# Performance work log

Measured on AMD Instinct MI355X. Metric: run time of the kernel, lower is better.

The kernel has to match this reference:

```python
import jax, jax.numpy as jnp
import numpy as np

E = 20000       # num edges (nodes of the edge-adjacency graph)
FDIM = 128      # edge_feature_dim
D = 16          # stalk_dim ('diagonal' => mlp output dim = D)
P = 300000      # number of adjacent (i, j) pairs extracted from L1
EPS = 1e-5      # LayerNorm eps


def _xavier(key, fan_in, fan_out):
    lim = np.sqrt(6.0 / (fan_in + fan_out)).astype(np.float32)
    return jax.random.uniform(key, (fan_in, fan_out), jnp.float32, -lim, lim)


def _layernorm(x, g, b):
    mu = jnp.mean(x, axis=-1, keepdims=True)
    var = jnp.mean((x - mu) ** 2, axis=-1, keepdims=True)
    return (x - mu) * jax.lax.rsqrt(var + EPS) * g + b


def setup_inputs() -> dict:
    key = jax.random.key(0)
    ks = jax.random.split(key, 8)
    return {
        "edge_features": jax.random.normal(ks[0], (E, FDIM), jnp.float32),
        "pair_i": jax.random.randint(ks[1], (P,), 0, E),
        "pair_j": jax.random.randint(ks[2], (P,), 0, E),
        # MLP: Linear(2F,64) -> LN -> ReLU -> Linear(64,32) -> LN -> ReLU -> Linear(32,D)
        "W1": _xavier(ks[3], 2 * FDIM, 64), "b1": jnp.zeros((64,), jnp.float32),
        "g1": jnp.ones((64,), jnp.float32), "be1": jnp.zeros((64,), jnp.float32),
        "W2": _xavier(ks[4], 64, 32), "b2": jnp.zeros((32,), jnp.float32),
        "g2": jnp.ones((32,), jnp.float32), "be2": jnp.zeros((32,), jnp.float32),
        "W3": _xavier(ks[5], 32, D), "b3": jnp.zeros((D,), jnp.float32),
    }


def reference(edge_features, pair_i, pair_j, W1, b1, g1, be1, W2, b2, g2, be2, W3, b3):
    # Gather the two edge feature vectors per adjacent pair and concat: [P, 2F]
    x = jnp.concatenate([edge_features[pair_i], edge_features[pair_j]], axis=1)
    h = jax.nn.relu(_layernorm(x @ W1 + b1, g1, be1))      # [P, 64]
    h = jax.nn.relu(_layernorm(h @ W2 + b2, g2, be2))      # [P, 32]
    params = h @ W3 + b3                                    # [P, D]
    # diagonal sheaf: F_ij = diag(params) for every pair, batched (diag_embed)
    return params[:, :, None] * jnp.eye(D, dtype=params.dtype)  # [P, D, D]
```

## Files before the change

### kernel.cpp

```cpp
#include <hip/hip_runtime.h>

__global__ void bad_map_marker(float* out) {
    if (threadIdx.x == 0 && blockIdx.x == 0) out[0] = 1.0e6f;
}

__device__ __forceinline__ void mlp_tail_compute(float* h, float* pr, int D,
        const float* g1, const float* be1,
        const float* W2, const float* b2,
        const float* g2, const float* be2,
        const float* W3, const float* b3) {
    float s = 0.f, ss = 0.f;
    #pragma unroll
    for (int d = 0; d < 64; ++d) { s += h[d]; ss += h[d] * h[d]; }
    float mu  = s * (1.f / 64.f);
    float inv = rsqrtf(ss * (1.f / 64.f) - mu * mu + 1e-5f);
    #pragma unroll
    for (int d = 0; d < 64; ++d)
        h[d] = fmaxf((h[d] - mu) * inv * g1[d] + be1[d], 0.f);

    float a2[32];
    const float4* w2v = (const float4*)W2;
    #pragma unroll
    for (int n = 0; n < 32; ++n) a2[n] = b2[n];
    for (int k = 0; k < 64; ++k) {
        float hk = h[k];
        #pragma unroll
        for (int q = 0; q < 8; ++q) {
            float4 w = w2v[k * 8 + q];
            a2[4 * q + 0] += hk * w.x;
            a2[4 * q + 1] += hk * w.y;
            a2[4 * q + 2] += hk * w.z;
            a2[4 * q + 3] += hk * w.w;
        }
    }
    s = 0.f; ss = 0.f;
    #pragma unroll
    for (int n = 0; n < 32; ++n) { s += a2[n]; ss += a2[n] * a2[n]; }
    mu  = s * (1.f / 32.f);
    inv = rsqrtf(ss * (1.f / 32.f) - mu * mu + 1e-5f);
    #pragma unroll
    for (int n = 0; n < 32; ++n)
        a2[n] = fmaxf((a2[n] - mu) * inv * g2[n] + be2[n], 0.f);

    for (int d = 0; d < D; ++d) pr[d] = b3[d];
    for (int k = 0; k < 32; ++k) {
        float hk = a2[k];
        const float* wr = W3 + k * D;
        for (int d = 0; d < D; ++d) pr[d] += hk * wr[d];
    }
}

__device__ __forceinline__ void store_diag16_f32_256(const float* pp, float* out, int P) {
    const int t = threadIdx.x;
    float4* outv = (float4*)out + (size_t)blockIdx.x * 16384;
    const int pbase = blockIdx.x * 256;
    #pragma unroll 8
    for (int it = 0; it < 64; ++it) {
        int g = it * 256 + t;
        int pl = g >> 6;
        int rem = g & 63;
        int d = rem >> 2;
        int c4 = rem & 3;
        float val = pp[pl * 17 + d];
        bool on = (d >> 2) == c4;
        float4 v;
        v.x = (on && (d & 3) == 0) ? val : 0.f;
        v.y = (on && (d & 3) == 1) ? val : 0.f;
        v.z = (on && (d & 3) == 2) ? val : 0.f;
        v.w = (on && (d & 3) == 3) ? val : 0.f;
        if (pbase + pl < P) outv[g] = v;
    }
}

__global__ __launch_bounds__(256)
void precompute_y(const float* __restrict__ ef, const float* __restrict__ W1,
                  const float* __restrict__ b1, float* __restrict__ Y, int E) {
    __shared__ __align__(16) float el[64 * 132];
    const int t = threadIdx.x;
    const int ebase = blockIdx.x * 64;

    for (int idx = t; idx < 2048; idx += 256) {
        int er = idx >> 5, ec = idx & 31;
        if (ebase + er < E)
            *((float4*)(el + er * 132) + ec) =
                *((const float4*)(ef + (size_t)(ebase + er) * 128) + ec);
    }
    __syncthreads();

    const int cg = t & 15;
    const int eg = t >> 4;
    const int half = cg >> 3;
    const int col64 = (cg & 7) * 8;

    float acc[4][8];
    #pragma unroll
    for (int i = 0; i < 4; ++i)
        #pragma unroll
        for (int c = 0; c < 8; ++c) acc[i][c] = 0.f;

    const float* wbase = W1 + (size_t)half * 128 * 64 + col64;
    #pragma unroll 4
    for (int k = 0; k < 128; ++k) {
        float4 w0 = *(const float4*)(wbase + (size_t)k * 64);
        float4 w1 = *(const float4*)(wbase + (size_t)k * 64 + 4);
        float wv[8] = {w0.x, w0.y, w0.z, w0.w, w1.x, w1.y, w1.z, w1.w};
        #pragma unroll
        for (int i = 0; i < 4; ++i) {
            float a = el[(eg * 4 + i) * 132 + k];
            #pragma unroll
            for (int c = 0; c < 8; ++c) acc[i][c] += a * wv[c];
        }
    }

    float bb[8];
    #pragma unroll
    for (int c = 0; c < 8; ++c) bb[c] = (half == 0) ? b1[col64 + c] : 0.f;
    #pragma unroll
    for (int i = 0; i < 4; ++i) {
        int e = ebase + eg * 4 + i;
        if (e < E) {
            float* dst = Y + (size_t)e * 128 + half * 64 + col64;
            #pragma unroll
            for (int c = 0; c < 8; ++c) dst[c] = acc[i][c] + bb[c];
        }
    }
}

__global__ __launch_bounds__(256)
void sheaf_pairs(const int* __restrict__ pi, const int* __restrict__ pj,
                 const float* __restrict__ Y,
                 const float* __restrict__ g1, const float* __restrict__ be1,
                 const float* __restrict__ W2, const float* __restrict__ b2,
                 const float* __restrict__ g2, const float* __restrict__ be2,
                 const float* __restrict__ W3, const float* __restrict__ b3,
                 float* __restrict__ out, int P) {
    __shared__ float pp[256 * 17];
    __shared__ __align__(16) float w2s[64 * 32];
    __shared__ __align__(16) float w3s[32 * 16];
    __shared__ float g1s[64], be1s[64], b2s[32], g2s[32], be2s[32], b3s[16];

    const int t = threadIdx.x;
    int p = blockIdx.x * 256 + t;
    int pc = p < P ? p : P - 1;
    int i = pi[pc], j = pj[pc];
    const float4* y1 = (const float4*)(Y + (size_t)i * 128);
    const float4* y2 = (const float4*)(Y + (size_t)j * 128 + 64);
    float h[64];
    #pragma unroll
    for (int q = 0; q < 16; ++q) {
        float4 a = y1[q], b = y2[q];
        h[4 * q + 0] = a.x + b.x;
        h[4 * q + 1] = a.y + b.y;
        h[4 * q + 2] = a.z + b.z;
        h[4 * q + 3] = a.w + b.w;
    }

    {
        const float4* s2 = (const float4*)W2;
        float4* d2 = (float4*)w2s;
        d2[t]       = s2[t];
        d2[t + 256] = s2[t + 256];
        if (t < 128) ((float4*)w3s)[t] = ((const float4*)W3)[t];
        if (t < 64)                 { g1s[t] = g1[t]; be1s[t] = be1[t]; }
        else if (t < 96)            b2s[t - 64]   = b2[t - 64];
        else if (t < 128)           g2s[t - 96]   = g2[t - 96];
        else if (t < 160)           be2s[t - 128] = be2[t - 128];
        else if (t < 176)           b3s[t - 160]  = b3[t - 160];
    }
    __syncthreads();

    float pr[16];
    mlp_tail_compute(h, pr, 16, g1s, be1s, w2s, b2s, g2s, be2s, w3s, b3s);
    #pragma unroll
    for (int d = 0; d < 16; ++d) pp[t * 17 + d] = pr[d];
    __syncthreads();
    store_diag16_f32_256(pp, out, P);
}

__global__ __launch_bounds__(256)
void sheaf_generic(const float* __restrict__ ef,
                   const int* __restrict__ pi, const int* __restrict__ pj,
                   const float* __restrict__ W1, const float* __restrict__ b1,
                   const float* __restrict__ g1, const float* __restrict__ be1,
                   const float* __restrict__ W2, const float* __restrict__ b2,
                   const float* __restrict__ g2, const float* __restrict__ be2,
                   const float* __restrict__ W3, const float* __restrict__ b3,
                   float* __restrict__ out, int P, int F, int D) {
    __shared__ float pp[256 * 17];
    int p = blockIdx.x * 256 + threadIdx.x;
    int pc = p < P ? p : P - 1;
    int i = pi[pc], j = pj[pc];
    const float* efi = ef + (size_t)i * F;
    const float* efj = ef + (size_t)j * F;
    float h[64];
    #pragma unroll
    for (int n = 0; n < 64; ++n) h[n] = b1[n];
    for (int k = 0; k < F; ++k) {
        float ei = efi[k];
        float ej = efj[k];
        const float* wi = W1 + (size_t)k * 64;
        const float* wj = W1 + (size_t)(F + k) * 64;
        #pragma unroll
        for (int n = 0; n < 64; ++n) h[n] += ei * wi[n] + ej * wj[n];
    }
    float pr[32];
    mlp_tail_compute(h, pr, D, g1, be1, W2, b2, g2, be2, W3, b3);

    if (D == 16) {
        #pragma unroll
        for (int d = 0; d < 16; ++d) pp[threadIdx.x * 17 + d] = pr[d];
        __syncthreads();
        store_diag16_f32_256(pp, out, P);
    } else {
        if (p < P) {
            float* po = out + (size_t)p * D * D;
            for (int r = 0; r < D; ++r) {
                float dv = pr[r];
                for (int c = 0; c < D; ++c) po[r * D + c] = (r == c) ? dv : 0.f;
            }
        }
    }
}

struct Map { int ef, pi, pj, w1, b1, g1, be1, w2, b2, g2, be2, w3, b3; };

static bool validate_map(const Map& m, const int* s, int n_in, long out_size,
                         int* Fo, int* Eo, int* Do, int* Po) {
    if (n_in < 13) return false;
    if (s[m.b1] != 64 || s[m.g1] != 64 || s[m.be1] != 64) return false;
    if (s[m.b2] != 32 || s[m.g2] != 32 || s[m.be2] != 32) return false;
    if (s[m.w2] != 64 * 32) return false;
    long w1 = s[m.w1];
    if (w1 <= 0 || (w1 % 128) != 0) return false;
    long F = w1 / 128;
    if (F <= 0) return false;
    int D = s[m.b3];
    if (D <= 0 || D > 32) return false;
    if (s[m.w3] != 32 * D) return false;
    long P = s[m.pi];
    if (P <= 0 || s[m.pj] != P) return false;
    long ef = s[m.ef];
    if (ef <= 0 || (ef % F) != 0) return false;
    long E = ef / F;
    if (out_size != P * D * D) return false;
    *Fo = (int)F; *Eo = (int)E; *Do = D; *Po = (int)P;
    return true;
}

extern "C" void kernel_launch(void* const* d_in, const int* in_sizes, int n_in,
                              void* d_out, int out_size, void* d_ws, size_t ws_size,
                              hipStream_t stream) {
    const Map pos   = {0, 1, 2, 3, 4, 5, 6, 7, 8, 9, 10, 11, 12};
    const Map alpha = {8, 11, 12, 0, 3, 9, 6, 1, 4, 10, 7, 2, 5};

    int F = 0, E = 0, D = 0, P = 0;
    Map m;
    if (validate_map(pos, in_sizes, n_in, (long)out_size, &F, &E, &D, &P)) {
        m = pos;
    } else if (validate_map(alpha, in_sizes, n_in, (long)out_size, &F, &E, &D, &P)) {
        m = alpha;
    } else {
        bad_map_marker<<<dim3(1), dim3(64), 0, stream>>>((float*)d_out);
        return;
    }

    const float* ef  = (const float*)d_in[m.ef];
    const int*   pi  = (const int*)d_in[m.pi];
    const int*   pj  = (const int*)d_in[m.pj];
    const float* W1  = (const float*)d_in[m.w1];
    const float* b1  = (const float*)d_in[m.b1];
    const float* g1  = (const float*)d_in[m.g1];
    const float* be1 = (const float*)d_in[m.be1];
    const float* W2  = (const float*)d_in[m.w2];
    const float* b2  = (const float*)d_in[m.b2];
    const float* g2  = (const float*)d_in[m.g2];
    const float* be2 = (const float*)d_in[m.be2];
    const float* W3  = (const float*)d_in[m.w3];
    const float* b3  = (const float*)d_in[m.b3];
    float* out = (float*)d_out;

    const size_t y_bytes = (size_t)E * 128 * 4;

    if (F == 128 && D == 16 && ws_size >= y_bytes) {
        float* Y = (float*)d_ws;
        precompute_y<<<dim3((E + 63) / 64), dim3(256), 0, stream>>>(ef, W1, b1, Y, E);
        sheaf_pairs<<<dim3((P + 255) / 256), dim3(256), 0, stream>>>(
            pi, pj, Y, g1, be1, W2, b2, g2, be2, W3, b3, out, P);
    } else {
        sheaf_generic<<<dim3((P + 255) / 256), dim3(256), 0, stream>>>(
            ef, pi, pj, W1, b1, g1, be1, W2, b2, g2, be2, W3, b3, out, P, F, D);
    }
}
```

Before: 389.4 us.

## Split each pair's MLP across four threads with shuffle reductions

Replaces the one-thread-per-pair MLP tail with a four-threads-per-pair layout. Each lane handles a 16-wide slice of the hidden layer and its part of the second matmul (against a transposed W2 in shared memory), and the partial sums and LayerNorm statistics are combined with XOR shuffles. Each lane then computes four outputs of the final layer, and the diagonal output is written as float4 stores. This cuts per-thread register pressure and raises occupancy and memory-level parallelism. In exchange it duplicates the second LayerNorm across lanes, adds shuffle traffic, and reloads the weight setup in four times as many blocks.

```diff
diff --git a/kernel.cpp b/kernel.cpp
--- a/kernel.cpp
+++ b/kernel.cpp
@@ -126,55 +126,118 @@
     }
 }
 
-__global__ __launch_bounds__(256)
-void sheaf_pairs(const int* __restrict__ pi, const int* __restrict__ pj,
-                 const float* __restrict__ Y,
-                 const float* __restrict__ g1, const float* __restrict__ be1,
-                 const float* __restrict__ W2, const float* __restrict__ b2,
-                 const float* __restrict__ g2, const float* __restrict__ be2,
-                 const float* __restrict__ W3, const float* __restrict__ b3,
-                 float* __restrict__ out, int P) {
-    __shared__ float pp[256 * 17];
-    __shared__ __align__(16) float w2s[64 * 32];
+__global__ __launch_bounds__(256, 4)
+void sheaf_pairs_quad(const int* __restrict__ pi, const int* __restrict__ pj,
+                      const float* __restrict__ Y,
+                      const float* __restrict__ g1, const float* __restrict__ be1,
+                      const float* __restrict__ W2, const float* __restrict__ b2,
+                      const float* __restrict__ g2, const float* __restrict__ be2,
+                      const float* __restrict__ W3, const float* __restrict__ b3,
+                      float* __restrict__ out, int P) {
+    __shared__ __align__(16) float w2t[32 * 64];
     __shared__ __align__(16) float w3s[32 * 16];
+    __shared__ __align__(16) float pp[64 * 20];
     __shared__ float g1s[64], be1s[64], b2s[32], g2s[32], be2s[32], b3s[16];
 
-    const int t = threadIdx.x;
-    int p = blockIdx.x * 256 + t;
+    const int t  = threadIdx.x;
+    const int pl = t >> 2;
+    const int q  = t & 3;
+    const int pbase = blockIdx.x * 64;
+    int p  = pbase + pl;
     int pc = p < P ? p : P - 1;
     int i = pi[pc], j = pj[pc];
-    const float4* y1 = (const float4*)(Y + (size_t)i * 128);
-    const float4* y2 = (const float4*)(Y + (size_t)j * 128 + 64);
-    float h[64];
-    #pragma unroll
-    for (int q = 0; q < 16; ++q) {
-        float4 a = y1[q], b = y2[q];
-        h[4 * q + 0] = a.x + b.x;
-        h[4 * q + 1] = a.y + b.y;
-        h[4 * q + 2] = a.z + b.z;
-        h[4 * q + 3] = a.w + b.w;
-    }
-
-    {
-        const float4* s2 = (const float4*)W2;
-        float4* d2 = (float4*)w2s;
-        d2[t]       = s2[t];
-        d2[t + 256] = s2[t + 256];
-        if (t < 128) ((float4*)w3s)[t] = ((const float4*)W3)[t];
-        if (t < 64)                 { g1s[t] = g1[t]; be1s[t] = be1[t]; }
-        else if (t < 96)            b2s[t - 64]   = b2[t - 64];
-        else if (t < 128)           g2s[t - 96]   = g2[t - 96];
-        else if (t < 160)           be2s[t - 128] = be2[t - 128];
-        else if (t < 176)           b3s[t - 160]  = b3[t - 160];
-    }
+
+    const int kbase = q * 16;
+    const float4* y1 = (const float4*)(Y + (size_t)i * 128 + kbase);
+    const float4* y2 = (const float4*)(Y + (size_t)j * 128 + 64 + kbase);
+    float4 ya0 = y1[0], ya1 = y1[1], ya2 = y1[2], ya3 = y1[3];
+    float4 yb0 = y2[0], yb1 = y2[1], yb2 = y2[2], yb3 = y2[3];
+
+    for (int idx = t; idx < 2048; idx += 256) {
+        int k = idx & 63, n = idx >> 6;
+        w2t[n * 64 + k] = W2[k * 32 + n];
+    }
+    if (t < 128) ((float4*)w3s)[t] = ((const float4*)W3)[t];
+    if (t < 64)                 { g1s[t] = g1[t]; be1s[t] = be1[t]; }
+    else if (t < 96)            b2s[t - 64]   = b2[t - 64];
+    else if (t < 128)           g2s[t - 96]   = g2[t - 96];
+    else if (t < 160)           be2s[t - 128] = be2[t - 128];
+    else if (t < 176)           b3s[t - 160]  = b3[t - 160];
     __syncthreads();
 
-    float pr[16];
-    mlp_tail_compute(h, pr, 16, g1s, be1s, w2s, b2s, g2s, be2s, w3s, b3s);
-    #pragma unroll
-    for (int d = 0; d < 16; ++d) pp[t * 17 + d] = pr[d];
+    float h[16];
+    h[ 0] = ya0.x + yb0.x; h[ 1] = ya0.y + yb0.y; h[ 2] = ya0.z + yb0.z; h[ 3] = ya0.w + yb0.w;
+    h[ 4] = ya1.x + yb1.x; h[ 5] = ya1.y + yb1.y; h[ 6] = ya1.z + yb1.z; h[ 7] = ya1.w + yb1.w;
+    h[ 8] = ya2.x + yb2.x; h[ 9] = ya2.y + yb2.y; h[10] = ya2.z + yb2.z; h[11] = ya2.w + yb2.w;
+    h[12] = ya3.x + yb3.x; h[13] = ya3.y + yb3.y; h[14] = ya3.z + yb3.z; h[15] = ya3.w + yb3.w;
+
+    float s = 0.f, ss = 0.f;
+    #pragma unroll
+    for (int d = 0; d < 16; ++d) { s += h[d]; ss += h[d] * h[d]; }
+    s  += __shfl_xor(s, 1);  ss += __shfl_xor(ss, 1);
+    s  += __shfl_xor(s, 2);  ss += __shfl_xor(ss, 2);
+    float mu  = s * (1.f / 64.f);
+    float inv = rsqrtf(ss * (1.f / 64.f) - mu * mu + 1e-5f);
+    #pragma unroll
+    for (int d = 0; d < 16; ++d)
+        h[d] = fmaxf((h[d] - mu) * inv * g1s[kbase + d] + be1s[kbase + d], 0.f);
+
+    float a2[32];
+    #pragma unroll
+    for (int n = 0; n < 32; ++n) {
+        const float4* wr = (const float4*)(w2t + n * 64 + kbase);
+        float4 w0 = wr[0], w1 = wr[1], w2f = wr[2], w3f = wr[3];
+        a2[n] = h[ 0] * w0.x + h[ 1] * w0.y + h[ 2] * w0.z + h[ 3] * w0.w
+              + h[ 4] * w1.x + h[ 5] * w1.y + h[ 6] * w1.z + h[ 7] * w1.w
+              + h[ 8] * w2f.x + h[ 9] * w2f.y + h[10] * w2f.z + h[11] * w2f.w
+              + h[12] * w3f.x + h[13] * w3f.y + h[14] * w3f.z + h[15] * w3f.w;
+    }
+    #pragma unroll
+    for (int n = 0; n < 32; ++n) {
+        a2[n] += __shfl_xor(a2[n], 1);
+        a2[n] += __shfl_xor(a2[n], 2);
+    }
+
+    s = 0.f; ss = 0.f;
+    #pragma unroll
+    for (int n = 0; n < 32; ++n) {
+        a2[n] += b2s[n];
+        s += a2[n]; ss += a2[n] * a2[n];
+    }
+    mu  = s * (1.f / 32.f);
+    inv = rsqrtf(ss * (1.f / 32.f) - mu * mu + 1e-5f);
+    #pragma unroll
+    for (int n = 0; n < 32; ++n)
+        a2[n] = fmaxf((a2[n] - mu) * inv * g2s[n] + be2s[n], 0.f);
+
+    const int n3 = q * 4;
+    float pr0 = b3s[n3 + 0], pr1 = b3s[n3 + 1], pr2 = b3s[n3 + 2], pr3 = b3s[n3 + 3];
+    #pragma unroll
+    for (int k = 0; k < 32; ++k) {
+        float4 w = *(const float4*)(w3s + k * 16 + n3);
+        float ak = a2[k];
+        pr0 += ak * w.x; pr1 += ak * w.y; pr2 += ak * w.z; pr3 += ak * w.w;
+    }
+    *(float4*)(pp + pl * 20 + n3) = make_float4(pr0, pr1, pr2, pr3);
     __syncthreads();
-    store_diag16_f32_256(pp, out, P);
+
+    float4* outv = (float4*)out + (size_t)blockIdx.x * 4096;
+    #pragma unroll 4
+    for (int it = 0; it < 16; ++it) {
+        int g = it * 256 + t;
+        int pl2 = g >> 6;
+        int rem = g & 63;
+        int d = rem >> 2;
+        int c4 = rem & 3;
+        float val = pp[pl2 * 20 + d];
+        bool on = (d >> 2) == c4;
+        float4 v;
+        v.x = (on && (d & 3) == 0) ? val : 0.f;
+        v.y = (on && (d & 3) == 1) ? val : 0.f;
+        v.z = (on && (d & 3) == 2) ? val : 0.f;
+        v.w = (on && (d & 3) == 3) ? val : 0.f;
+        if (pbase + pl2 < P) outv[g] = v;
+    }
 }
 
 __global__ __launch_bounds__(256)
@@ -284,7 +347,7 @@
     if (F == 128 && D == 16 && ws_size >= y_bytes) {
         float* Y = (float*)d_ws;
         precompute_y<<<dim3((E + 63) / 64), dim3(256), 0, stream>>>(ef, W1, b1, Y, E);
-        sheaf_pairs<<<dim3((P + 255) / 256), dim3(256), 0, stream>>>(
+        sheaf_pairs_quad<<<dim3((P + 63) / 64), dim3(256), 0, stream>>>(
             pi, pj, Y, g1, be1, W2, b2, g2, be2, W3, b3, out, P);
     } else {
         sheaf_generic<<<dim3((P + 255) / 256), dim3(256), 0, stream>>>(
```

Result: slower. 406.2 us (+4.3%).

## Stream layer-1 activations from gathered Y to cut registers and raise occupancy

Applied to the files above, without the earlier changes.

The pair kernel no longer holds all 64 hidden values in registers. It makes one pass over the gathered Y rows to compute the LayerNorm statistics, then reloads them to apply the norm and accumulate the second layer inline, and it hints launch bounds for 4 blocks per CU. The gathers are moved after the weight staging so they overlap it. The Y precompute uses 32 edges per block instead of 64, giving more blocks. The cost is reading the gathered Y rows twice, which relies on them being served from cache.

```diff
diff --git a/kernel.cpp b/kernel.cpp
--- a/kernel.cpp
+++ b/kernel.cpp
@@ -75,11 +75,11 @@
 __global__ __launch_bounds__(256)
 void precompute_y(const float* __restrict__ ef, const float* __restrict__ W1,
                   const float* __restrict__ b1, float* __restrict__ Y, int E) {
-    __shared__ __align__(16) float el[64 * 132];
+    __shared__ __align__(16) float el[32 * 132];
     const int t = threadIdx.x;
-    const int ebase = blockIdx.x * 64;
-
-    for (int idx = t; idx < 2048; idx += 256) {
+    const int ebase = blockIdx.x * 32;
+
+    for (int idx = t; idx < 1024; idx += 256) {
         int er = idx >> 5, ec = idx & 31;
         if (ebase + er < E)
             *((float4*)(el + er * 132) + ec) =
@@ -92,9 +92,9 @@
     const int half = cg >> 3;
     const int col64 = (cg & 7) * 8;
 
-    float acc[4][8];
-    #pragma unroll
-    for (int i = 0; i < 4; ++i)
+    float acc[2][8];
+    #pragma unroll
+    for (int i = 0; i < 2; ++i)
         #pragma unroll
         for (int c = 0; c < 8; ++c) acc[i][c] = 0.f;
 
@@ -105,8 +105,8 @@
         float4 w1 = *(const float4*)(wbase + (size_t)k * 64 + 4);
         float wv[8] = {w0.x, w0.y, w0.z, w0.w, w1.x, w1.y, w1.z, w1.w};
         #pragma unroll
-        for (int i = 0; i < 4; ++i) {
-            float a = el[(eg * 4 + i) * 132 + k];
+        for (int i = 0; i < 2; ++i) {
+            float a = el[(eg * 2 + i) * 132 + k];
             #pragma unroll
             for (int c = 0; c < 8; ++c) acc[i][c] += a * wv[c];
         }
@@ -116,8 +116,8 @@
     #pragma unroll
     for (int c = 0; c < 8; ++c) bb[c] = (half == 0) ? b1[col64 + c] : 0.f;
     #pragma unroll
-    for (int i = 0; i < 4; ++i) {
-        int e = ebase + eg * 4 + i;
+    for (int i = 0; i < 2; ++i) {
+        int e = ebase + eg * 2 + i;
         if (e < E) {
             float* dst = Y + (size_t)e * 128 + half * 64 + col64;
             #pragma unroll
@@ -126,7 +126,7 @@
     }
 }
 
-__global__ __launch_bounds__(256)
+__global__ __launch_bounds__(256, 4)
 void sheaf_pairs(const int* __restrict__ pi, const int* __restrict__ pj,
                  const float* __restrict__ Y,
                  const float* __restrict__ g1, const float* __restrict__ be1,
@@ -140,20 +140,6 @@
     __shared__ float g1s[64], be1s[64], b2s[32], g2s[32], be2s[32], b3s[16];
 
     const int t = threadIdx.x;
-    int p = blockIdx.x * 256 + t;
-    int pc = p < P ? p : P - 1;
-    int i = pi[pc], j = pj[pc];
-    const float4* y1 = (const float4*)(Y + (size_t)i * 128);
-    const float4* y2 = (const float4*)(Y + (size_t)j * 128 + 64);
-    float h[64];
-    #pragma unroll
-    for (int q = 0; q < 16; ++q) {
-        float4 a = y1[q], b = y2[q];
-        h[4 * q + 0] = a.x + b.x;
-        h[4 * q + 1] = a.y + b.y;
-        h[4 * q + 2] = a.z + b.z;
-        h[4 * q + 3] = a.w + b.w;
-    }
 
     {
         const float4* s2 = (const float4*)W2;
@@ -167,10 +153,74 @@
         else if (t < 160)           be2s[t - 128] = be2[t - 128];
         else if (t < 176)           b3s[t - 160]  = b3[t - 160];
     }
+
+    int p = blockIdx.x * 256 + t;
+    int pc = p < P ? p : P - 1;
+    int i = pi[pc], j = pj[pc];
+    const float4* y1 = (const float4*)(Y + (size_t)i * 128);
+    const float4* y2 = (const float4*)(Y + (size_t)j * 128 + 64);
+
+    float s = 0.f, ss = 0.f;
+    #pragma unroll
+    for (int q = 0; q < 16; ++q) {
+        float4 a = y1[q], b = y2[q];
+        float h0 = a.x + b.x, h1 = a.y + b.y, h2 = a.z + b.z, h3 = a.w + b.w;
+        s  += h0 + h1 + h2 + h3;
+        ss += h0 * h0 + h1 * h1 + h2 * h2 + h3 * h3;
+    }
+    float mu  = s * (1.f / 64.f);
+    float inv = rsqrtf(ss * (1.f / 64.f) - mu * mu + 1e-5f);
+
     __syncthreads();
 
+    float a2[32];
+    #pragma unroll
+    for (int n = 0; n < 32; ++n) a2[n] = b2s[n];
+    #pragma unroll
+    for (int q = 0; q < 16; ++q) {
+        float4 a = y1[q], b = y2[q];
+        float hh[4] = {a.x + b.x, a.y + b.y, a.z + b.z, a.w + b.w};
+        #pragma unroll
+        for (int c = 0; c < 4; ++c) {
+            int k = 4 * q + c;
+            float hk = fmaxf((hh[c] - mu) * inv * g1s[k] + be1s[k], 0.f);
+            const float4* wr = (const float4*)(w2s + k * 32);
+            #pragma unroll
+            for (int u = 0; u < 8; ++u) {
+                float4 w = wr[u];
+                a2[4 * u + 0] += hk * w.x;
+                a2[4 * u + 1] += hk * w.y;
+                a2[4 * u + 2] += hk * w.z;
+                a2[4 * u + 3] += hk * w.w;
+            }
+        }
+    }
+
+    s = 0.f; ss = 0.f;
+    #pragma unroll
+    for (int n = 0; n < 32; ++n) { s += a2[n]; ss += a2[n] * a2[n]; }
+    mu  = s * (1.f / 32.f);
+    inv = rsqrtf(ss * (1.f / 32.f) - mu * mu + 1e-5f);
+    #pragma unroll
+    for (int n = 0; n < 32; ++n)
+        a2[n] = fmaxf((a2[n] - mu) * inv * g2s[n] + be2s[n], 0.f);
+
     float pr[16];
-    mlp_tail_compute(h, pr, 16, g1s, be1s, w2s, b2s, g2s, be2s, w3s, b3s);
+    #pragma unroll
+    for (int d = 0; d < 16; ++d) pr[d] = b3s[d];
+    #pragma unroll 8
+    for (int k = 0; k < 32; ++k) {
+        float hk = a2[k];
+        #pragma unroll
+        for (int u = 0; u < 4; ++u) {
+            float4 w = *(const float4*)(w3s + k * 16 + u * 4);
+            pr[4 * u + 0] += hk * w.x;
+            pr[4 * u + 1] += hk * w.y;
+            pr[4 * u + 2] += hk * w.z;
+            pr[4 * u + 3] += hk * w.w;
+        }
+    }
+
     #pragma unroll
     for (int d = 0; d < 16; ++d) pp[t * 17 + d] = pr[d];
     __syncthreads();
@@ -283,7 +333,7 @@
 
     if (F == 128 && D == 16 && ws_size >= y_bytes) {
         float* Y = (float*)d_ws;
-        precompute_y<<<dim3((E + 63) / 64), dim3(256), 0, stream>>>(ef, W1, b1, Y, E);
+        precompute_y<<<dim3((E + 31) / 32), dim3(256), 0, stream>>>(ef, W1, b1, Y, E);
         sheaf_pairs<<<dim3((P + 255) / 256), dim3(256), 0, stream>>>(
             pi, pj, Y, g1, be1, W2, b2, g2, be2, W3, b3, out, P);
     } else {
```

Measured after the change: 708.5 us. 1.82x slower.
